# Kernel tuning notes

Measured on AMD Instinct MI355X. Metric: run time of the kernel, lower is better.

## Reference

```python
import jax, jax.numpy as jnp
import numpy as np

B, S, D_IN, D, H, HD, HALF, L = 64, 500, 64, 128, 8, 16, 5, 2
WIN = 2 * HALF + 1  # 11 attended positions per query
EPS = 1e-12  # HF layer_norm_eps default


def _ln(x, g, b):
    m = x.mean(-1, keepdims=True)
    v = ((x - m) ** 2).mean(-1, keepdims=True)
    return (x - m) / jnp.sqrt(v + EPS) * g + b


def setup_inputs() -> dict:
    key = jax.random.key(0)
    ks = jax.random.split(key, 24)
    n = lambda i, shape: jax.random.normal(ks[i], shape, jnp.float32) * 0.02
    return {
        "x": jax.random.normal(ks[0], (B, S, D_IN), jnp.float32),
        "W_in": n(1, (D_IN, D)), "b_in": jnp.zeros((D,), jnp.float32),
        "pos_emb": n(2, (512, D)), "tt_emb": n(3, (D,)),
        "ln_emb_g": jnp.ones((D,), jnp.float32), "ln_emb_b": jnp.zeros((D,), jnp.float32),
        "Wq": n(4, (L, D, D)), "bq": jnp.zeros((L, D), jnp.float32),
        "Wk": n(5, (L, D, D)), "bk": jnp.zeros((L, D), jnp.float32),
        "Wv": n(6, (L, D, D)), "bv": jnp.zeros((L, D), jnp.float32),
        "Wo": n(7, (L, D, D)), "bo": jnp.zeros((L, D), jnp.float32),
        "ln1_g": jnp.ones((L, D), jnp.float32), "ln1_b": jnp.zeros((L, D), jnp.float32),
        "Wi": n(8, (L, D, 512)), "bi": jnp.zeros((L, 512), jnp.float32),
        "Wo2": n(9, (L, 512, D)), "bo2": jnp.zeros((L, D), jnp.float32),
        "ln2_g": jnp.ones((L, D), jnp.float32), "ln2_b": jnp.zeros((L, D), jnp.float32),
        "W_cls": n(10, (D, 2)), "b_cls": jnp.zeros((2,), jnp.float32),
    }


def reference(x, W_in, b_in, pos_emb, tt_emb, ln_emb_g, ln_emb_b,
              Wq, bq, Wk, bk, Wv, bv, Wo, bo, ln1_g, ln1_b,
              Wi, bi, Wo2, bo2, ln2_g, ln2_b, W_cls, b_cls):
    # input projection + RoBERTa-style embeddings (position ids start at padding_idx+1=2)
    h = x @ W_in + b_in
    pos_ids = 2 + jnp.arange(S)
    h = _ln(h + pos_emb[pos_ids] + tt_emb, ln_emb_g, ln_emb_b)

    # sliding-window gather indices: each query attends [i-HALF, i+HALF]
    idx = jnp.arange(S)[:, None] + jnp.arange(-HALF, HALF + 1)[None, :]
    valid = (idx >= 0) & (idx < S)
    idxc = jnp.clip(idx, 0, S - 1)
    scale = 1.0 / jnp.sqrt(jnp.float32(HD))

    for l in range(L):
        qh = (h @ Wq[l] + bq[l]).reshape(B, S, H, HD).transpose(0, 2, 1, 3)
        kh = (h @ Wk[l] + bk[l]).reshape(B, S, H, HD).transpose(0, 2, 1, 3)
        vh = (h @ Wv[l] + bv[l]).reshape(B, S, H, HD).transpose(0, 2, 1, 3)
        kk = kh[:, :, idxc]
        scores = jnp.einsum('bhsd,bhswd->bhsw', qh * scale, kk)
        scores = jnp.where(valid, scores, -jnp.inf)
        probs = jax.nn.softmax(scores, axis=-1)
        vv = vh[:, :, idxc]
        ctx = jnp.einsum('bhsw,bhswd->bhsd', probs, vv)
        ctx = ctx.transpose(0, 2, 1, 3).reshape(B, S, D)
        h = _ln(ctx @ Wo[l] + bo[l] + h, ln1_g[l], ln1_b[l])
        ff = jax.nn.gelu(h @ Wi[l] + bi[l], approximate=False) @ Wo2[l] + bo2[l]
        h = _ln(ff + h, ln2_g[l], ln2_b[l])

    pooled = h.mean(axis=1)  # mean over sequence
    return pooled @ W_cls + b_cls
```

## Files before the change

kernel.cpp:

```cpp
#include <hip/hip_runtime.h>
#include <hip/hip_bf16.h>
#include <math.h>

#define BB 64
#define SS 500
#define DIN 64
#define DD 128
#define HH 8
#define HDIM 16
#define HALF_ 5
#define WINW 11
#define LL 2
#define FF 512
#define MM (BB*SS)
#define LN_EPS 1e-12f

typedef __attribute__((ext_vector_type(8))) short short8;
typedef __attribute__((ext_vector_type(4))) float f32x4;

__global__ __launch_bounds__(256) void k_prep(
    const float* __restrict__ Wq, const float* __restrict__ Wk,
    const float* __restrict__ Wv, const float* __restrict__ Wo,
    const float* __restrict__ Wi, const float* __restrict__ Wo2,
    const float* __restrict__ Win, __hip_bfloat16* __restrict__ wT)
{
    const int m = blockIdx.y;
    const float* src; int Kd, Nd, kshift, doff;
    if (m == 12) {
        src = Win; Kd = 64; Nd = 128; kshift = 6; doff = 393216;
    } else {
        const int l = m / 6, t = m % 6;
        int toff;
        switch (t) {
          case 0:  src = Wq  + l*16384; Kd=128; Nd=128; kshift=7; toff=0;      break;
          case 1:  src = Wk  + l*16384; Kd=128; Nd=128; kshift=7; toff=16384;  break;
          case 2:  src = Wv  + l*16384; Kd=128; Nd=128; kshift=7; toff=32768;  break;
          case 3:  src = Wo  + l*16384; Kd=128; Nd=128; kshift=7; toff=49152;  break;
          case 4:  src = Wi  + l*65536; Kd=128; Nd=512; kshift=7; toff=65536;  break;
          default: src = Wo2 + l*65536; Kd=512; Nd=128; kshift=9; toff=131072; break;
        }
        doff = l*196608 + toff;
    }
    __hip_bfloat16* dst = wT + doff;
    const int NK = Kd * Nd;
    int e = (blockIdx.x * 256 + threadIdx.x) * 4;
    if (e >= NK) return;
    #pragma unroll
    for (int j = 0; j < 4; ++j, ++e) {
        int n = e >> kshift, kx = e & (Kd - 1);
        dst[(size_t)n * Kd + kx] = __float2bfloat16(src[(size_t)kx * Nd + n]);
    }
}

__global__ __launch_bounds__(256) void k_xcvt(
    const float* __restrict__ x, __hip_bfloat16* __restrict__ xbf)
{
    int i = (blockIdx.x * 256 + threadIdx.x) * 4;
    if (i >= MM * DIN) return;
    float4 v = *(const float4*)(x + i);
    ushort4 o;
    __hip_bfloat16 t0 = __float2bfloat16(v.x); o.x = *(unsigned short*)&t0;
    __hip_bfloat16 t1 = __float2bfloat16(v.y); o.y = *(unsigned short*)&t1;
    __hip_bfloat16 t2 = __float2bfloat16(v.z); o.z = *(unsigned short*)&t2;
    __hip_bfloat16 t3 = __float2bfloat16(v.w); o.w = *(unsigned short*)&t3;
    *(ushort4*)(xbf + i) = o;
}

#define GEMM_MAIN(Abf, lda, Kdim, WTbf, ldw, n0w)                             \
    __shared__ __align__(16) __hip_bfloat16 As[64][72];                       \
    __shared__ __align__(16) __hip_bfloat16 Ws[128][72];                      \
    const int tid = threadIdx.x;                                              \
    const int wid = tid >> 6;                                                 \
    const int l15 = tid & 15;                                                 \
    const int l4  = (tid & 63) >> 4;                                          \
    const int m0  = blockIdx.x * 64;                                          \
    f32x4 acc[8];                                                             \
    _Pragma("unroll")                                                         \
    for (int n = 0; n < 8; ++n) acc[n] = (f32x4){0.f, 0.f, 0.f, 0.f};         \
    for (int k0 = 0; k0 < (Kdim); k0 += 64) {                                 \
        _Pragma("unroll")                                                     \
        for (int it = 0; it < 2; ++it) {                                      \
            int lin = it * 2048 + tid * 8;                                    \
            int r = lin >> 6, c = lin & 63;                                   \
            *(uint4*)&As[r][c] =                                              \
                *(const uint4*)((Abf) + (size_t)(m0 + r) * (lda) + k0 + c);   \
        }                                                                     \
        _Pragma("unroll")                                                     \
        for (int it = 0; it < 4; ++it) {                                      \
            int lin = it * 2048 + tid * 8;                                    \
            int r = lin >> 6, c = lin & 63;                                   \
            *(uint4*)&Ws[r][c] =                                              \
                *(const uint4*)((WTbf) + (size_t)((n0w) + r) * (ldw) + k0 + c); \
        }                                                                     \
        __syncthreads();                                                      \
        _Pragma("unroll")                                                     \
        for (int kc = 0; kc < 64; kc += 32) {                                 \
            short8 a0 = *(const short8*)&As[wid * 16 + l15][kc + l4 * 8];     \
            _Pragma("unroll")                                                 \
            for (int n = 0; n < 8; ++n) {                                     \
                short8 bf = *(const short8*)&Ws[n * 16 + l15][kc + l4 * 8];   \
                acc[n] = __builtin_amdgcn_mfma_f32_16x16x32_bf16(a0, bf, acc[n], 0, 0, 0); \
            }                                                                 \
        }                                                                     \
        __syncthreads();                                                      \
    }

__global__ __launch_bounds__(256, 4) void k_embed(
    const __hip_bfloat16* __restrict__ xbf, const __hip_bfloat16* __restrict__ wInT,
    const float* __restrict__ bin, const float* __restrict__ pos,
    const float* __restrict__ tt, const float* __restrict__ g,
    const float* __restrict__ be, float* __restrict__ h,
    __hip_bfloat16* __restrict__ hbf)
{
    GEMM_MAIN(xbf, DIN, DIN, wInT, DIN, 0)
    #pragma unroll
    for (int qq = 0; qq < 4; ++qq) {
        const int row = m0 + wid * 16 + l4 * 4 + qq;
        const int s = row % SS;
        float vals[8]; float s1 = 0.f, s2 = 0.f;
        #pragma unroll
        for (int n = 0; n < 8; ++n) {
            const int col = n * 16 + l15;
            float val = acc[n][qq] + bin[col] + tt[col] + pos[(size_t)(2 + s) * DD + col];
            vals[n] = val; s1 += val; s2 += val * val;
        }
        #pragma unroll
        for (int o = 1; o < 16; o <<= 1) {
            s1 += __shfl_xor(s1, o, 16);
            s2 += __shfl_xor(s2, o, 16);
        }
        const float mean = s1 * (1.0f / DD);
        const float var  = s2 * (1.0f / DD) - mean * mean;
        const float rstd = rsqrtf(var + LN_EPS);
        #pragma unroll
        for (int n = 0; n < 8; ++n) {
            const int col = n * 16 + l15;
            const float o = (vals[n] - mean) * rstd * g[col] + be[col];
            h[(size_t)row * DD + col]   = o;
            hbf[(size_t)row * DD + col] = __float2bfloat16(o);
        }
    }
}

__global__ __launch_bounds__(256) void k_fused(
    const __hip_bfloat16* __restrict__ hin,
    const __hip_bfloat16* __restrict__ wTq, const __hip_bfloat16* __restrict__ wTk,
    const __hip_bfloat16* __restrict__ wTv, const __hip_bfloat16* __restrict__ wTo,
    const float* __restrict__ bq, const float* __restrict__ bk,
    const float* __restrict__ bv, const float* __restrict__ bo,
    const float* __restrict__ hres,
    const float* __restrict__ g1, const float* __restrict__ bt1,
    float* __restrict__ hout, __hip_bfloat16* __restrict__ hbfout)
{
    __shared__ __align__(16) char smem[49472];
    __hip_bfloat16* kS   = (__hip_bfloat16*)smem;
    __hip_bfloat16* vS   = (__hip_bfloat16*)(smem + 13056);
    __hip_bfloat16* hS   = (__hip_bfloat16*)(smem + 26112);
    __hip_bfloat16* qS   = (__hip_bfloat16*)(smem + 39168);
    float*          pS   = (float*)(smem + 47872);
    float*          rsum = (float*)(smem + 48960);
    __hip_bfloat16* ctxS = hS;

    const int tid = threadIdx.x;
    const int wid = tid >> 6, l15 = tid & 15, l4 = (tid & 63) >> 4;
    const int b = blockIdx.y;
    const int s0 = blockIdx.x * 32;

    #pragma unroll
    for (int it = 0; it < 3; ++it) {
        int lin = it * 256 + tid;
        int r = lin >> 4, c8 = (lin & 15) * 8;
        int s = s0 - 5 + r;
        uint4 val = {0, 0, 0, 0};
        if (s >= 0 && s < SS)
            val = *(const uint4*)(hin + ((size_t)(b * SS + s)) * DD + c8);
        *(uint4*)&hS[r * 136 + c8] = val;
    }
    __syncthreads();

    for (int j = wid; j < 9; j += 4) {
        const int out = j / 3, rt = j % 3;
        const __hip_bfloat16* WT = (out == 0) ? wTq : ((out == 1) ? wTk : wTv);
        const float* bias = (out == 0) ? bq : ((out == 1) ? bk : bv);
        for (int n = 0; n < 8; ++n) {
            f32x4 a = (f32x4){0.f, 0.f, 0.f, 0.f};
            #pragma unroll
            for (int kc = 0; kc < 4; ++kc) {
                short8 af  = *(const short8*)&hS[(rt * 16 + l15) * 136 + kc * 32 + l4 * 8];
                short8 bfg = *(const short8*)(WT + (size_t)(n * 16 + l15) * DD + kc * 32 + l4 * 8);
                a = __builtin_amdgcn_mfma_f32_16x16x32_bf16(af, bfg, a, 0, 0, 0);
            }
            const int col = n * 16 + l15;
            const float bcol = bias[col];
            #pragma unroll
            for (int qq = 0; qq < 4; ++qq) {
                const int row = rt * 16 + l4 * 4 + qq;
                const float val = a[qq] + bcol;
                if (out == 0) {
                    if (row >= 5 && row < 37)
                        qS[(row - 5) * 136 + col] = __float2bfloat16(val * 0.25f);
                } else if (out == 1) {
                    kS[row * 136 + col] = __float2bfloat16(val);
                } else {
                    vS[row * 136 + col] = __float2bfloat16(val);
                }
            }
        }
    }
    __syncthreads();

    {
        const int g = tid >> 4, wl = tid & 15;
        for (int qh = 0; qh < 2; ++qh) {
            const int qrow = qh * 16 + g;
            const int sq = s0 + qrow;
            const int sk = sq + wl - HALF_;
            const bool valid = (wl < WINW) && (sq < SS) && (sk >= 0) && (sk < SS);
            #pragma unroll
            for (int hh = 0; hh < 8; ++hh) {
                const int off = hh * 16;
                float sc = 0.f;
                const unsigned* qp = (const unsigned*)&qS[qrow * 136 + off];
                const unsigned* kp = (const unsigned*)&kS[(qrow + wl) * 136 + off];
                #pragma unroll
                for (int d2 = 0; d2 < 8; ++d2) {
                    unsigned qu = qp[d2], ku = kp[d2];
                    sc += __uint_as_float(qu << 16) * __uint_as_float(ku << 16)
                        + __uint_as_float(qu & 0xffff0000u) * __uint_as_float(ku & 0xffff0000u);
                }
                sc = valid ? sc : -INFINITY;
                float mx = sc;
                #pragma unroll
                for (int o = 1; o < 16; o <<= 1) mx = fmaxf(mx, __shfl_xor(mx, o, 16));
                float p = valid ? __expf(sc - mx) : 0.f;
                float den = p;
                #pragma unroll
                for (int o = 1; o < 16; o <<= 1) den += __shfl_xor(den, o, 16);
                const float inv = (den > 0.f) ? 1.f / den : 0.f;
                pS[g * 17 + wl] = p;
                float cd = 0.f;
                #pragma unroll
                for (int w2 = 0; w2 < WINW; ++w2)
                    cd += pS[g * 17 + w2] * __bfloat162float(vS[(qrow + w2) * 136 + off + wl]);
                ctxS[qrow * 136 + off + wl] = __float2bfloat16(cd * inv);
            }
        }
    }
    __syncthreads();

    const int rt2 = wid & 1, nh = wid >> 1;
    f32x4 ac[4];
    #pragma unroll
    for (int n4 = 0; n4 < 4; ++n4) {
        ac[n4] = (f32x4){0.f, 0.f, 0.f, 0.f};
        const int n = nh * 4 + n4;
        #pragma unroll
        for (int kc = 0; kc < 4; ++kc) {
            short8 af  = *(const short8*)&ctxS[(rt2 * 16 + l15) * 136 + kc * 32 + l4 * 8];
            short8 bfg = *(const short8*)(wTo + (size_t)(n * 16 + l15) * DD + kc * 32 + l4 * 8);
            ac[n4] = __builtin_amdgcn_mfma_f32_16x16x32_bf16(af, bfg, ac[n4], 0, 0, 0);
        }
    }
    float vals[4][4];
    #pragma unroll
    for (int qq = 0; qq < 4; ++qq) {
        const int r16 = l4 * 4 + qq;
        const int qrow = rt2 * 16 + r16;
        const int sq = s0 + qrow;
        const bool vr = (sq < SS);
        float s1 = 0.f, s2 = 0.f;
        #pragma unroll
        for (int n4 = 0; n4 < 4; ++n4) {
            const int col = (nh * 4 + n4) * 16 + l15;
            const float resv = vr ? hres[((size_t)(b * SS + sq)) * DD + col] : 0.f;
            const float val = ac[n4][qq] + bo[col] + resv;
            vals[qq][n4] = val; s1 += val; s2 += val * val;
        }
        #pragma unroll
        for (int o = 1; o < 16; o <<= 1) {
            s1 += __shfl_xor(s1, o, 16);
            s2 += __shfl_xor(s2, o, 16);
        }
        if (l15 == 0) {
            rsum[rt2 * 64 + nh * 32 + r16 * 2]     = s1;
            rsum[rt2 * 64 + nh * 32 + r16 * 2 + 1] = s2;
        }
    }
    __syncthreads();
    #pragma unroll
    for (int qq = 0; qq < 4; ++qq) {
        const int r16 = l4 * 4 + qq;
        const int qrow = rt2 * 16 + r16;
        const int sq = s0 + qrow;
        if (sq >= SS) continue;
        const float S1 = rsum[rt2 * 64 + r16 * 2]     + rsum[rt2 * 64 + 32 + r16 * 2];
        const float S2 = rsum[rt2 * 64 + r16 * 2 + 1] + rsum[rt2 * 64 + 32 + r16 * 2 + 1];
        const float mean = S1 * (1.0f / DD);
        const float var  = S2 * (1.0f / DD) - mean * mean;
        const float rstd = rsqrtf(var + LN_EPS);
        #pragma unroll
        for (int n4 = 0; n4 < 4; ++n4) {
            const int col = (nh * 4 + n4) * 16 + l15;
            const float o = (vals[qq][n4] - mean) * rstd * g1[col] + bt1[col];
            hout[((size_t)(b * SS + sq)) * DD + col]   = o;
            hbfout[((size_t)(b * SS + sq)) * DD + col] = __float2bfloat16(o);
        }
    }
}

__global__ __launch_bounds__(256, 4) void k_gemm_gelu(
    const __hip_bfloat16* __restrict__ hbf,
    const __hip_bfloat16* __restrict__ wTi,
    const float* __restrict__ bias, __hip_bfloat16* __restrict__ hid)
{
    const int n0g = blockIdx.y * 128;
    GEMM_MAIN(hbf, DD, DD, wTi, DD, n0g)
    #pragma unroll
    for (int qq = 0; qq < 4; ++qq) {
        const int row = m0 + wid * 16 + l4 * 4 + qq;
        #pragma unroll
        for (int n = 0; n < 8; ++n) {
            const int col = n0g + n * 16 + l15;
            float val = acc[n][qq] + bias[col];
            val = 0.5f * val * (1.f + erff(val * 0.70710678118f));
            hid[(size_t)row * FF + col] = __float2bfloat16(val);
        }
    }
}

__global__ __launch_bounds__(256, 4) void k_gemm_lnres(
    const __hip_bfloat16* __restrict__ Abf, int lda, int Kdim,
    const __hip_bfloat16* __restrict__ WT,
    const float* __restrict__ bias, const float* __restrict__ res,
    const float* __restrict__ g, const float* __restrict__ bt,
    float* __restrict__ outF, __hip_bfloat16* __restrict__ outB)
{
    GEMM_MAIN(Abf, lda, Kdim, WT, Kdim, 0)
    #pragma unroll
    for (int qq = 0; qq < 4; ++qq) {
        const int row = m0 + wid * 16 + l4 * 4 + qq;
        float vals[8]; float s1 = 0.f, s2 = 0.f;
        #pragma unroll
        for (int n = 0; n < 8; ++n) {
            const int col = n * 16 + l15;
            float val = acc[n][qq] + bias[col] + res[(size_t)row * DD + col];
            vals[n] = val; s1 += val; s2 += val * val;
        }
        #pragma unroll
        for (int o = 1; o < 16; o <<= 1) {
            s1 += __shfl_xor(s1, o, 16);
            s2 += __shfl_xor(s2, o, 16);
        }
        const float mean = s1 * (1.0f / DD);
        const float var  = s2 * (1.0f / DD) - mean * mean;
        const float rstd = rsqrtf(var + LN_EPS);
        #pragma unroll
        for (int n = 0; n < 8; ++n) {
            const int col = n * 16 + l15;
            const float o = (vals[n] - mean) * rstd * g[col] + bt[col];
            outF[(size_t)row * DD + col] = o;
            outB[(size_t)row * DD + col] = __float2bfloat16(o);
        }
    }
}

__global__ __launch_bounds__(128) void k_final(
    const float* __restrict__ h, const float* __restrict__ Wc,
    const float* __restrict__ bc, float* __restrict__ out)
{
    const int b = blockIdx.x, d = threadIdx.x;
    float p = 0.f;
    for (int s = 0; s < SS; ++s) p += h[((size_t)(b * SS + s)) * DD + d];
    p *= (1.0f / SS);
    float l0 = p * Wc[d * 2 + 0];
    float l1 = p * Wc[d * 2 + 1];
    #pragma unroll
    for (int off = 1; off < 64; off <<= 1) {
        l0 += __shfl_xor(l0, off);
        l1 += __shfl_xor(l1, off);
    }
    __shared__ float r[2][2];
    const int wid = d >> 6;
    if ((d & 63) == 0) { r[wid][0] = l0; r[wid][1] = l1; }
    __syncthreads();
    if (d == 0) {
        out[b * 2 + 0] = r[0][0] + r[1][0] + bc[0];
        out[b * 2 + 1] = r[0][1] + r[1][1] + bc[1];
    }
}

extern "C" void kernel_launch(void* const* d_in, const int* in_sizes, int n_in,
                              void* d_out, int out_size, void* d_ws, size_t ws_size,
                              hipStream_t stream)
{
    const float* x      = (const float*)d_in[0];
    const float* W_in   = (const float*)d_in[1];
    const float* b_in   = (const float*)d_in[2];
    const float* pos    = (const float*)d_in[3];
    const float* tt     = (const float*)d_in[4];
    const float* lng    = (const float*)d_in[5];
    const float* lnb    = (const float*)d_in[6];
    const float* Wq     = (const float*)d_in[7];
    const float* bq     = (const float*)d_in[8];
    const float* Wk     = (const float*)d_in[9];
    const float* bk     = (const float*)d_in[10];
    const float* Wv     = (const float*)d_in[11];
    const float* bv     = (const float*)d_in[12];
    const float* Wo     = (const float*)d_in[13];
    const float* bo     = (const float*)d_in[14];
    const float* ln1g   = (const float*)d_in[15];
    const float* ln1b   = (const float*)d_in[16];
    const float* Wi     = (const float*)d_in[17];
    const float* bi     = (const float*)d_in[18];
    const float* Wo2    = (const float*)d_in[19];
    const float* bo2    = (const float*)d_in[20];
    const float* ln2g   = (const float*)d_in[21];
    const float* ln2b   = (const float*)d_in[22];
    const float* Wc     = (const float*)d_in[23];
    const float* bc     = (const float*)d_in[24];

    float*          ws   = (float*)d_ws;
    float*          hA   = ws;
    __hip_bfloat16* hbA  = (__hip_bfloat16*)(ws + 4096000);
    __hip_bfloat16* xbf  = (__hip_bfloat16*)(ws + 6144000);
    __hip_bfloat16* wT   = (__hip_bfloat16*)(ws + 7168000);
    __hip_bfloat16* hid  = (__hip_bfloat16*)(ws + 7368704);
    float*          hB   = ws + 15560704;
    __hip_bfloat16* hbB  = (__hip_bfloat16*)(ws + 19656704);

    k_prep<<<dim3(64, 13), 256, 0, stream>>>(Wq, Wk, Wv, Wo, Wi, Wo2, W_in, wT);
    k_xcvt<<<2000, 256, 0, stream>>>(x, xbf);
    k_embed<<<MM / 64, 256, 0, stream>>>(xbf, wT + 393216, b_in, pos, tt, lng, lnb,
                                         hA, hbA);

    float* hI = hA; __hip_bfloat16* hbI = hbA;
    float* hO = hB; __hip_bfloat16* hbO = hbB;
    for (int l = 0; l < LL; ++l) {
        const __hip_bfloat16* wTq  = wT + l * 196608;
        const __hip_bfloat16* wTk  = wTq + 16384;
        const __hip_bfloat16* wTv  = wTq + 32768;
        const __hip_bfloat16* wTo  = wTq + 49152;
        const __hip_bfloat16* wTi  = wTq + 65536;
        const __hip_bfloat16* wTo2 = wTq + 131072;

        k_fused<<<dim3(16, BB), 256, 0, stream>>>(
            hbI, wTq, wTk, wTv, wTo,
            bq + l * DD, bk + l * DD, bv + l * DD, bo + l * DD,
            hI, ln1g + l * DD, ln1b + l * DD, hO, hbO);

        k_gemm_gelu<<<dim3(MM / 64, 4), 256, 0, stream>>>(
            hbO, wTi, bi + l * FF, hid);

        k_gemm_lnres<<<dim3(MM / 64, 1), 256, 0, stream>>>(
            hid, FF, FF, wTo2, bo2 + l * DD, hO, ln2g + l * DD, ln2b + l * DD,
            hO, hbO);

        float* tf = hI; hI = hO; hO = tf;
        __hip_bfloat16* tb = hbI; hbI = hbO; hbO = tb;
    }

    k_final<<<BB, 128, 0, stream>>>(hI, Wc, bc, (float*)d_out);
}
```

Before: 394.0 us.

## Double k_fused block to 512 threads and redistribute QKV, attention and out-proj work

The fused attention kernel now launches 512 threads per block instead of 256. The QKV projection is split into 72 independent 16x16 output tiles spread over 8 waves. The attention stage assigns one query row per 16-lane group instead of looping over two, and each wave of the output projection computes 2 column tiles instead of 4. LayerNorm partial sums are reduced across 4 column groups through a larger shared buffer. The aim is more waves per CU to hide LDS and global latency within the same shared-memory footprint per block, at the cost of extra register pressure from the launch bound and a little more reduction work.

```diff
diff --git a/kernel.cpp b/kernel.cpp
--- a/kernel.cpp
+++ b/kernel.cpp
@@ -142,7 +142,7 @@
     }
 }
 
-__global__ __launch_bounds__(256) void k_fused(
+__global__ __launch_bounds__(512, 4) void k_fused(
     const __hip_bfloat16* __restrict__ hin,
     const __hip_bfloat16* __restrict__ wTq, const __hip_bfloat16* __restrict__ wTk,
     const __hip_bfloat16* __restrict__ wTv, const __hip_bfloat16* __restrict__ wTo,
@@ -152,58 +152,63 @@
     const float* __restrict__ g1, const float* __restrict__ bt1,
     float* __restrict__ hout, __hip_bfloat16* __restrict__ hbfout)
 {
-    __shared__ __align__(16) char smem[49472];
+    __shared__ __align__(16) char smem[51072];
     __hip_bfloat16* kS   = (__hip_bfloat16*)smem;
     __hip_bfloat16* vS   = (__hip_bfloat16*)(smem + 13056);
     __hip_bfloat16* hS   = (__hip_bfloat16*)(smem + 26112);
     __hip_bfloat16* qS   = (__hip_bfloat16*)(smem + 39168);
     float*          pS   = (float*)(smem + 47872);
-    float*          rsum = (float*)(smem + 48960);
+    float*          rsum = (float*)(smem + 50048);
     __hip_bfloat16* ctxS = hS;
 
     const int tid = threadIdx.x;
-    const int wid = tid >> 6, l15 = tid & 15, l4 = (tid & 63) >> 4;
+    const int wid = tid >> 6;
+    const int l15 = tid & 15, l4 = (tid & 63) >> 4;
     const int b = blockIdx.y;
     const int s0 = blockIdx.x * 32;
 
     #pragma unroll
-    for (int it = 0; it < 3; ++it) {
-        int lin = it * 256 + tid;
-        int r = lin >> 4, c8 = (lin & 15) * 8;
-        int s = s0 - 5 + r;
-        uint4 val = {0, 0, 0, 0};
-        if (s >= 0 && s < SS)
-            val = *(const uint4*)(hin + ((size_t)(b * SS + s)) * DD + c8);
-        *(uint4*)&hS[r * 136 + c8] = val;
+    for (int it = 0; it < 2; ++it) {
+        int lin = it * 512 + tid;
+        if (lin < 768) {
+            int r = lin >> 4, c8 = (lin & 15) * 8;
+            int s = s0 - 5 + r;
+            uint4 val = {0, 0, 0, 0};
+            if (s >= 0 && s < SS)
+                val = *(const uint4*)(hin + ((size_t)(b * SS + s)) * DD + c8);
+            *(uint4*)&hS[r * 136 + c8] = val;
+        }
     }
     __syncthreads();
 
-    for (int j = wid; j < 9; j += 4) {
-        const int out = j / 3, rt = j % 3;
+    #pragma unroll
+    for (int i = 0; i < 9; ++i) {
+        const int t = wid + i * 8;
+        const int out = t / 24;
+        const int rem = t - out * 24;
+        const int rt = rem >> 3, n = rem & 7;
         const __hip_bfloat16* WT = (out == 0) ? wTq : ((out == 1) ? wTk : wTv);
         const float* bias = (out == 0) ? bq : ((out == 1) ? bk : bv);
-        for (int n = 0; n < 8; ++n) {
-            f32x4 a = (f32x4){0.f, 0.f, 0.f, 0.f};
-            #pragma unroll
-            for (int kc = 0; kc < 4; ++kc) {
-                short8 af  = *(const short8*)&hS[(rt * 16 + l15) * 136 + kc * 32 + l4 * 8];
-                short8 bfg = *(const short8*)(WT + (size_t)(n * 16 + l15) * DD + kc * 32 + l4 * 8);
-                a = __builtin_amdgcn_mfma_f32_16x16x32_bf16(af, bfg, a, 0, 0, 0);
-            }
-            const int col = n * 16 + l15;
-            const float bcol = bias[col];
-            #pragma unroll
-            for (int qq = 0; qq < 4; ++qq) {
-                const int row = rt * 16 + l4 * 4 + qq;
-                const float val = a[qq] + bcol;
-                if (out == 0) {
-                    if (row >= 5 && row < 37)
-                        qS[(row - 5) * 136 + col] = __float2bfloat16(val * 0.25f);
-                } else if (out == 1) {
-                    kS[row * 136 + col] = __float2bfloat16(val);
-                } else {
-                    vS[row * 136 + col] = __float2bfloat16(val);
-                }
+        f32x4 a = (f32x4){0.f, 0.f, 0.f, 0.f};
+        #pragma unroll
+        for (int kc = 0; kc < 4; ++kc) {
+            short8 af  = *(const short8*)&hS[(rt * 16 + l15) * 136 + kc * 32 + l4 * 8];
+            short8 bfg = *(const short8*)(WT + (size_t)(n * 16 + l15) * DD + kc * 32 + l4 * 8);
+            a = __builtin_amdgcn_mfma_f32_16x16x32_bf16(af, bfg, a, 0, 0, 0);
+        }
+        const int col = n * 16 + l15;
+        const float bcol = bias[col];
+        #pragma unroll
+        for (int qq = 0; qq < 4; ++qq) {
+            const int row = rt * 16 + l4 * 4 + qq;
+            const float val = a[qq] + bcol;
+            if (out == 0) {
+                if (row >= 5 && row < 37)
+                    qS[(row - 5) * 136 + col] = __float2bfloat16(val * 0.25f);
+            } else if (out == 1) {
+                kS[row * 136 + col] = __float2bfloat16(val);
+            } else {
+                vS[row * 136 + col] = __float2bfloat16(val);
             }
         }
     }
@@ -211,49 +216,46 @@
 
     {
         const int g = tid >> 4, wl = tid & 15;
-        for (int qh = 0; qh < 2; ++qh) {
-            const int qrow = qh * 16 + g;
-            const int sq = s0 + qrow;
-            const int sk = sq + wl - HALF_;
-            const bool valid = (wl < WINW) && (sq < SS) && (sk >= 0) && (sk < SS);
+        const int sq = s0 + g;
+        const int sk = sq + wl - HALF_;
+        const bool valid = (wl < WINW) && (sq < SS) && (sk >= 0) && (sk < SS);
+        #pragma unroll
+        for (int hh = 0; hh < 8; ++hh) {
+            const int off = hh * 16;
+            float sc = 0.f;
+            const unsigned* qp = (const unsigned*)&qS[g * 136 + off];
+            const unsigned* kp = (const unsigned*)&kS[(g + wl) * 136 + off];
             #pragma unroll
-            for (int hh = 0; hh < 8; ++hh) {
-                const int off = hh * 16;
-                float sc = 0.f;
-                const unsigned* qp = (const unsigned*)&qS[qrow * 136 + off];
-                const unsigned* kp = (const unsigned*)&kS[(qrow + wl) * 136 + off];
-                #pragma unroll
-                for (int d2 = 0; d2 < 8; ++d2) {
-                    unsigned qu = qp[d2], ku = kp[d2];
-                    sc += __uint_as_float(qu << 16) * __uint_as_float(ku << 16)
-                        + __uint_as_float(qu & 0xffff0000u) * __uint_as_float(ku & 0xffff0000u);
-                }
-                sc = valid ? sc : -INFINITY;
-                float mx = sc;
-                #pragma unroll
-                for (int o = 1; o < 16; o <<= 1) mx = fmaxf(mx, __shfl_xor(mx, o, 16));
-                float p = valid ? __expf(sc - mx) : 0.f;
-                float den = p;
-                #pragma unroll
-                for (int o = 1; o < 16; o <<= 1) den += __shfl_xor(den, o, 16);
-                const float inv = (den > 0.f) ? 1.f / den : 0.f;
-                pS[g * 17 + wl] = p;
-                float cd = 0.f;
-                #pragma unroll
-                for (int w2 = 0; w2 < WINW; ++w2)
-                    cd += pS[g * 17 + w2] * __bfloat162float(vS[(qrow + w2) * 136 + off + wl]);
-                ctxS[qrow * 136 + off + wl] = __float2bfloat16(cd * inv);
+            for (int d2 = 0; d2 < 8; ++d2) {
+                unsigned qu = qp[d2], ku = kp[d2];
+                sc += __uint_as_float(qu << 16) * __uint_as_float(ku << 16)
+                    + __uint_as_float(qu & 0xffff0000u) * __uint_as_float(ku & 0xffff0000u);
             }
+            sc = valid ? sc : -INFINITY;
+            float mx = sc;
+            #pragma unroll
+            for (int o = 1; o < 16; o <<= 1) mx = fmaxf(mx, __shfl_xor(mx, o, 16));
+            float p = valid ? __expf(sc - mx) : 0.f;
+            float den = p;
+            #pragma unroll
+            for (int o = 1; o < 16; o <<= 1) den += __shfl_xor(den, o, 16);
+            const float inv = (den > 0.f) ? 1.f / den : 0.f;
+            pS[g * 17 + wl] = p;
+            float cd = 0.f;
+            #pragma unroll
+            for (int w2 = 0; w2 < WINW; ++w2)
+                cd += pS[g * 17 + w2] * __bfloat162float(vS[(g + w2) * 136 + off + wl]);
+            ctxS[g * 136 + off + wl] = __float2bfloat16(cd * inv);
         }
     }
     __syncthreads();
 
     const int rt2 = wid & 1, nh = wid >> 1;
-    f32x4 ac[4];
-    #pragma unroll
-    for (int n4 = 0; n4 < 4; ++n4) {
+    f32x4 ac[2];
+    #pragma unroll
+    for (int n4 = 0; n4 < 2; ++n4) {
         ac[n4] = (f32x4){0.f, 0.f, 0.f, 0.f};
-        const int n = nh * 4 + n4;
+        const int n = nh * 2 + n4;
         #pragma unroll
         for (int kc = 0; kc < 4; ++kc) {
             short8 af  = *(const short8*)&ctxS[(rt2 * 16 + l15) * 136 + kc * 32 + l4 * 8];
@@ -261,7 +263,7 @@
             ac[n4] = __builtin_amdgcn_mfma_f32_16x16x32_bf16(af, bfg, ac[n4], 0, 0, 0);
         }
     }
-    float vals[4][4];
+    float vals[4][2];
     #pragma unroll
     for (int qq = 0; qq < 4; ++qq) {
         const int r16 = l4 * 4 + qq;
@@ -270,8 +272,8 @@
         const bool vr = (sq < SS);
         float s1 = 0.f, s2 = 0.f;
         #pragma unroll
-        for (int n4 = 0; n4 < 4; ++n4) {
-            const int col = (nh * 4 + n4) * 16 + l15;
+        for (int n4 = 0; n4 < 2; ++n4) {
+            const int col = (nh * 2 + n4) * 16 + l15;
             const float resv = vr ? hres[((size_t)(b * SS + sq)) * DD + col] : 0.f;
             const float val = ac[n4][qq] + bo[col] + resv;
             vals[qq][n4] = val; s1 += val; s2 += val * val;
@@ -282,8 +284,8 @@
             s2 += __shfl_xor(s2, o, 16);
         }
         if (l15 == 0) {
-            rsum[rt2 * 64 + nh * 32 + r16 * 2]     = s1;
-            rsum[rt2 * 64 + nh * 32 + r16 * 2 + 1] = s2;
+            rsum[((rt2 * 4 + nh) * 16 + r16) * 2]     = s1;
+            rsum[((rt2 * 4 + nh) * 16 + r16) * 2 + 1] = s2;
         }
     }
     __syncthreads();
@@ -293,14 +295,18 @@
         const int qrow = rt2 * 16 + r16;
         const int sq = s0 + qrow;
         if (sq >= SS) continue;
-        const float S1 = rsum[rt2 * 64 + r16 * 2]     + rsum[rt2 * 64 + 32 + r16 * 2];
-        const float S2 = rsum[rt2 * 64 + r16 * 2 + 1] + rsum[rt2 * 64 + 32 + r16 * 2 + 1];
+        float S1 = 0.f, S2 = 0.f;
+        #pragma unroll
+        for (int j = 0; j < 4; ++j) {
+            S1 += rsum[((rt2 * 4 + j) * 16 + r16) * 2];
+            S2 += rsum[((rt2 * 4 + j) * 16 + r16) * 2 + 1];
+        }
         const float mean = S1 * (1.0f / DD);
         const float var  = S2 * (1.0f / DD) - mean * mean;
         const float rstd = rsqrtf(var + LN_EPS);
         #pragma unroll
-        for (int n4 = 0; n4 < 4; ++n4) {
-            const int col = (nh * 4 + n4) * 16 + l15;
+        for (int n4 = 0; n4 < 2; ++n4) {
+            const int col = (nh * 2 + n4) * 16 + l15;
             const float o = (vals[qq][n4] - mean) * rstd * g1[col] + bt1[col];
             hout[((size_t)(b * SS + sq)) * DD + col]   = o;
             hbfout[((size_t)(b * SS + sq)) * DD + col] = __float2bfloat16(o);
@@ -443,7 +449,7 @@
         const __hip_bfloat16* wTi  = wTq + 65536;
         const __hip_bfloat16* wTo2 = wTq + 131072;
 
-        k_fused<<<dim3(16, BB), 256, 0, stream>>>(
+        k_fused<<<dim3(16, BB), 512, 0, stream>>>(
             hbI, wTq, wTk, wTv, wTo,
             bq + l * DD, bk + l * DD, bv + l * DD, bo + l * DD,
             hI, ln1g + l * DD, ln1b + l * DD, hO, hbO);
```

New measurement: 336.8 us. 1.17x faster.
